# Optimization experiments

Measured on AMD Instinct MI355X. Metric: run time of the kernel, lower is better.

Reference implementation:

```python
import jax, jax.numpy as jnp
import numpy as np

N = 100000
E = 3200000
IN_DIM = 256
HID = 128
OUT_DIM = 64


def setup_inputs() -> dict:
    key = jax.random.key(0)
    ks = jax.random.split(key, 8)
    features = jax.random.normal(ks[0], (N, IN_DIM), dtype=jnp.float32)
    edge_row = jax.random.randint(ks[1], (E,), 0, N, dtype=jnp.int32)
    edge_col = jax.random.randint(ks[2], (E,), 0, N, dtype=jnp.int32)
    edge_val = jax.random.uniform(ks[3], (E,), dtype=jnp.float32)
    W1 = jax.random.normal(ks[4], (IN_DIM, HID), dtype=jnp.float32) * (1.0 / np.sqrt(IN_DIM))
    b1 = jnp.zeros((HID,), dtype=jnp.float32)
    W2 = jax.random.normal(ks[5], (HID, OUT_DIM), dtype=jnp.float32) * (1.0 / np.sqrt(HID))
    b2 = jnp.zeros((OUT_DIM,), dtype=jnp.float32)
    return {"features": features, "edge_row": edge_row, "edge_col": edge_col,
            "edge_val": edge_val, "W1": W1, "b1": b1, "W2": W2, "b2": b2}


def reference(features, edge_row, edge_col, edge_val, W1, b1, W2, b2):
    # fc1: [N, IN_DIM] @ [IN_DIM, HID] + b1
    h = features @ W1 + b1                                   # [N, HID]
    # spmm(A, h): for each edge (r, c, v): out[r] += v * h[c]
    msgs = edge_val[:, None] * h[edge_col]                    # [E, HID] gather
    h = jax.ops.segment_sum(msgs, edge_row, num_segments=N)   # [N, HID] scatter-add
    h = jax.nn.relu(h)
    h = h @ W2 + b2                                           # [N, OUT_DIM]
    return jax.nn.log_softmax(h, axis=1)
```

## Files before the change

### kernel.cpp

```cpp
#include <hip/hip_runtime.h>
#include <math.h>

constexpr int IN_DIM  = 256;
constexpr int HID     = 128;
constexpr int OUT_DIM = 64;

constexpr int BROWS   = 128;
constexpr int NBUCK   = 782;
constexpr int CAP     = 4608;
constexpr int CHUNK   = 8192;

typedef short  bf16x8 __attribute__((ext_vector_type(8)));
typedef float  f32x4  __attribute__((ext_vector_type(4)));

__device__ __forceinline__ unsigned short f2bf(float x) {
    union { float f; unsigned u; } v; v.f = x;
    unsigned r = v.u + 0x7FFF + ((v.u >> 16) & 1);
    return (unsigned short)(r >> 16);
}

__global__ __launch_bounds__(256) void w1t_kernel(const float* __restrict__ W1,
                                                  unsigned short* __restrict__ W1T)
{
    int idx = blockIdx.x * 256 + threadIdx.x;
    int k = idx >> 7;
    int n = idx & 127;
    W1T[n * IN_DIM + k] = f2bf(W1[idx]);
}

__global__ __launch_bounds__(256) void w2t_kernel(const float* __restrict__ W2,
                                                  unsigned short* __restrict__ W2T)
{
    int idx = blockIdx.x * 256 + threadIdx.x;
    int k = idx >> 6;
    int n = idx & 63;
    W2T[n * HID + k] = f2bf(W2[idx]);
}

constexpr int PADK = 264;

__global__ __launch_bounds__(256) void fc1_mfma(const float* __restrict__ feat,
                                                const unsigned short* __restrict__ W1T,
                                                const float* __restrict__ b1,
                                                unsigned short* __restrict__ h1b, int N)
{
    __shared__ unsigned short sA[64 * PADK];
    const int t    = threadIdx.x;
    const int lane = t & 63;
    const int w    = t >> 6;
    const int quad = lane >> 4;
    const int ln15 = lane & 15;
    const int row0 = blockIdx.x * 64;

#pragma unroll
    for (int i = 0; i < 16; ++i) {
        int flat = i * 256 + t;
        int r    = flat >> 6;
        int k4   = flat & 63;
        int gr   = row0 + r;
        float4 v = make_float4(0.f, 0.f, 0.f, 0.f);
        if (gr < N)
            v = *(const float4*)&feat[(size_t)gr * IN_DIM + k4 * 4];
        ushort4 o;
        o.x = f2bf(v.x); o.y = f2bf(v.y); o.z = f2bf(v.z); o.w = f2bf(v.w);
        *(ushort4*)&sA[r * PADK + k4 * 4] = o;
    }
    __syncthreads();

    f32x4 acc[8];
#pragma unroll
    for (int i = 0; i < 8; ++i) acc[i] = (f32x4){0.f, 0.f, 0.f, 0.f};

#pragma unroll
    for (int ks = 0; ks < 8; ++ks) {
        bf16x8 afrag = *(const bf16x8*)&sA[(w * 16 + ln15) * PADK + ks * 32 + quad * 8];
#pragma unroll
        for (int nt = 0; nt < 8; ++nt) {
            bf16x8 bfrag = *(const bf16x8*)&W1T[(size_t)(nt * 16 + ln15) * IN_DIM + ks * 32 + quad * 8];
            acc[nt] = __builtin_amdgcn_mfma_f32_16x16x32_bf16(afrag, bfrag, acc[nt], 0, 0, 0);
        }
    }

#pragma unroll
    for (int nt = 0; nt < 8; ++nt) {
        int col = nt * 16 + ln15;
        float bias = b1[col];
#pragma unroll
        for (int r = 0; r < 4; ++r) {
            int grow = row0 + w * 16 + quad * 4 + r;
            if (grow < N)
                h1b[(size_t)grow * HID + col] = f2bf(acc[nt][r] + bias);
        }
    }
}

__global__ __launch_bounds__(256) void bin_kernel(const int* __restrict__ erow,
                                                  const int* __restrict__ ecol,
                                                  const float* __restrict__ eval,
                                                  int* __restrict__ gCursor,
                                                  int2* __restrict__ binned, int E)
{
    __shared__ int sCnt[NBUCK];
    __shared__ int sBase[NBUCK];
    const int t = threadIdx.x;
    const int e0 = blockIdx.x * CHUNK;
    const int eEnd = min(e0 + CHUNK, E);

    for (int i = t; i < NBUCK; i += 256) sCnt[i] = 0;
    __syncthreads();

    for (int e = e0 + t; e < eEnd; e += 256)
        atomicAdd(&sCnt[erow[e] >> 7], 1);
    __syncthreads();

    for (int i = t; i < NBUCK; i += 256) {
        int c = sCnt[i];
        sBase[i] = c ? atomicAdd(&gCursor[i], c) : 0;
        sCnt[i] = 0;
    }
    __syncthreads();

    for (int e = e0 + t; e < eEnd; e += 256) {
        int   r = erow[e];
        int   c = ecol[e];
        float v = eval[e];
        int   b = r >> 7;
        int off = sBase[b] + atomicAdd(&sCnt[b], 1);
        if (off < CAP)
            binned[(size_t)b * CAP + off] = make_int2((c << 8) | ((r & 127) << 25),
                                                      __float_as_int(v));
    }
}

__global__ __launch_bounds__(256) void sort_bucket2(const int* __restrict__ gCursor,
                                                    const int2* __restrict__ binned,
                                                    int2* __restrict__ edges2,
                                                    int2* __restrict__ rowIdx, int N)
{
    __shared__ int sHist[BROWS];
    __shared__ int sStart[BROWS + 1];
    __shared__ int sCur[BROWS];
    const int t  = threadIdx.x;
    const int b  = blockIdx.x;
    const int nE = min(gCursor[b], CAP);
    const size_t base = (size_t)b * CAP;

    if (t < BROWS) sHist[t] = 0;
    __syncthreads();

    for (int i = t; i < nE; i += 256)
        atomicAdd(&sHist[(unsigned)binned[base + i].x >> 25], 1);
    __syncthreads();

    if (t < BROWS) sStart[t + 1] = sHist[t];
    if (t == 0) sStart[0] = 0;
    __syncthreads();
    for (int o = 1; o < BROWS; o <<= 1) {
        int v = 0;
        if (t < BROWS) {
            v = sStart[t + 1];
            if (t >= o) v += sStart[t + 1 - o];
        }
        __syncthreads();
        if (t < BROWS) sStart[t + 1] = v;
        __syncthreads();
    }
    if (t < BROWS) sCur[t] = sStart[t];
    __syncthreads();

    for (int i = t; i < nE; i += 256) {
        int2 p = binned[base + i];
        int rl = (unsigned)p.x >> 25;
        int pos = atomicAdd(&sCur[rl], 1);
        edges2[base + pos] = p;
    }

    if (t < BROWS) {
        int r = b * BROWS + t;
        if (r < N)
            rowIdx[r] = make_int2((int)base + sStart[t], (int)base + sStart[t + 1]);
    }
}

__device__ __forceinline__ void accum_row(const int2* __restrict__ edges2,
                                          const char* __restrict__ h1base,
                                          int j, int jend, int lane4,
                                          float& ax, float& ay)
{
    ax = 0.f; ay = 0.f;
    for (; j + 7 < jend; j += 8) {
        int2 p[8];
#pragma unroll
        for (int u = 0; u < 8; ++u) p[u] = edges2[j + u];
        unsigned g[8];
#pragma unroll
        for (int u = 0; u < 8; ++u)
            g[u] = *(const unsigned*)(h1base + ((p[u].x & 0x01FFFFFF) + lane4));
#pragma unroll
        for (int u = 0; u < 8; ++u) {
            float v = __int_as_float(p[u].y);
            ax += v * __uint_as_float(g[u] << 16);
            ay += v * __uint_as_float(g[u] & 0xFFFF0000u);
        }
    }
    for (; j < jend; ++j) {
        int2 p = edges2[j];
        unsigned g = *(const unsigned*)(h1base + ((p.x & 0x01FFFFFF) + lane4));
        float v = __int_as_float(p.y);
        ax += v * __uint_as_float(g << 16);
        ay += v * __uint_as_float(g & 0xFFFF0000u);
    }
}

__global__ __launch_bounds__(256) void spmm_kernel(const int2* __restrict__ rowIdx,
                                                   const int2* __restrict__ edges2,
                                                   const unsigned short* __restrict__ h1b,
                                                   unsigned* __restrict__ h2b, int N)
{
    const int lane  = threadIdx.x & 63;
    const int lane4 = lane * 4;
    const int wv    = (blockIdx.x * blockDim.x + threadIdx.x) >> 6;
    const int r0    = wv * 2;
    const int r1    = r0 + 1;
    if (r0 >= N) return;
    const char* h1base = (const char*)h1b;

    float ax0, ay0;
    int2 se0 = rowIdx[r0];
    accum_row(edges2, h1base, se0.x, se0.y, lane4, ax0, ay0);
    ax0 = fmaxf(ax0, 0.f); ay0 = fmaxf(ay0, 0.f);
    h2b[(size_t)r0 * 64 + lane] = (unsigned)f2bf(ax0) | ((unsigned)f2bf(ay0) << 16);

    if (r1 < N) {
        float ax1, ay1;
        int2 se1 = rowIdx[r1];
        accum_row(edges2, h1base, se1.x, se1.y, lane4, ax1, ay1);
        ax1 = fmaxf(ax1, 0.f); ay1 = fmaxf(ay1, 0.f);
        h2b[(size_t)r1 * 64 + lane] = (unsigned)f2bf(ax1) | ((unsigned)f2bf(ay1) << 16);
    }
}

__global__ __launch_bounds__(256) void fc2_mfma(const unsigned short* __restrict__ h2b,
                                                const unsigned short* __restrict__ W2T,
                                                const float* __restrict__ b2,
                                                float* __restrict__ out, int N)
{
    const int t    = threadIdx.x;
    const int lane = t & 63;
    const int w    = t >> 6;
    const int quad = lane >> 4;
    const int ln15 = lane & 15;
    const int row0 = blockIdx.x * 64;

    int arow = row0 + w * 16 + ln15;
    if (arow >= N) arow = N - 1;

    f32x4 acc[4];
#pragma unroll
    for (int i = 0; i < 4; ++i) acc[i] = (f32x4){0.f, 0.f, 0.f, 0.f};

#pragma unroll
    for (int ks = 0; ks < 4; ++ks) {
        bf16x8 afrag = *(const bf16x8*)&h2b[(size_t)arow * HID + ks * 32 + quad * 8];
#pragma unroll
        for (int nt = 0; nt < 4; ++nt) {
            bf16x8 bfrag = *(const bf16x8*)&W2T[(size_t)(nt * 16 + ln15) * HID + ks * 32 + quad * 8];
            acc[nt] = __builtin_amdgcn_mfma_f32_16x16x32_bf16(afrag, bfrag, acc[nt], 0, 0, 0);
        }
    }

    float bias[4];
#pragma unroll
    for (int nt = 0; nt < 4; ++nt) bias[nt] = b2[nt * 16 + ln15];

#pragma unroll
    for (int r = 0; r < 4; ++r) {
        float v[4];
#pragma unroll
        for (int nt = 0; nt < 4; ++nt) v[nt] = acc[nt][r] + bias[nt];

        float m = fmaxf(fmaxf(v[0], v[1]), fmaxf(v[2], v[3]));
#pragma unroll
        for (int o = 1; o < 16; o <<= 1) m = fmaxf(m, __shfl_xor(m, o));
        float s = __expf(v[0] - m) + __expf(v[1] - m) +
                  __expf(v[2] - m) + __expf(v[3] - m);
#pragma unroll
        for (int o = 1; o < 16; o <<= 1) s += __shfl_xor(s, o);
        float ls = __logf(s);

        int grow = row0 + w * 16 + quad * 4 + r;
        if (grow < N) {
#pragma unroll
            for (int nt = 0; nt < 4; ++nt)
                out[(size_t)grow * OUT_DIM + nt * 16 + ln15] = v[nt] - m - ls;
        }
    }
}

extern "C" void kernel_launch(void* const* d_in, const int* in_sizes, int n_in,
                              void* d_out, int out_size, void* d_ws, size_t ws_size,
                              hipStream_t stream) {
    const float* feat = (const float*)d_in[0];
    const int*   erow = (const int*)d_in[1];
    const int*   ecol = (const int*)d_in[2];
    const float* eval = (const float*)d_in[3];
    const float* W1   = (const float*)d_in[4];
    const float* b1   = (const float*)d_in[5];
    const float* W2   = (const float*)d_in[6];
    const float* b2   = (const float*)d_in[7];
    float*       out  = (float*)d_out;

    const int N = in_sizes[0] / IN_DIM;
    const int E = in_sizes[1];

    unsigned short* h1b    = (unsigned short*)d_ws;
    unsigned short* h2b    = h1b + (size_t)N * HID;
    int2*           binned = (int2*)(h2b + (size_t)N * HID);
    int2*           edges2 = binned + (size_t)NBUCK * CAP;
    int2*           rowIdx = edges2 + (size_t)NBUCK * CAP;
    unsigned short* W1T    = (unsigned short*)(rowIdx + N);
    unsigned short* W2T    = W1T + IN_DIM * HID;
    int*            gCursor= (int*)(W2T + HID * OUT_DIM);

    hipMemsetAsync(gCursor, 0, NBUCK * sizeof(int), stream);

    w1t_kernel<<<(IN_DIM * HID) / 256, 256, 0, stream>>>(W1, W1T);
    w2t_kernel<<<(HID * OUT_DIM) / 256, 256, 0, stream>>>(W2, W2T);
    fc1_mfma<<<(N + 63) / 64, 256, 0, stream>>>(feat, W1T, b1, h1b, N);
    bin_kernel<<<(E + CHUNK - 1) / CHUNK, 256, 0, stream>>>(erow, ecol, eval,
                                                            gCursor, binned, E);
    sort_bucket2<<<NBUCK, 256, 0, stream>>>(gCursor, binned, edges2, rowIdx, N);

    const int nwaves = (N + 1) / 2;
    const int nblk   = (nwaves + 3) / 4;
    spmm_kernel<<<nblk, 256, 0, stream>>>(rowIdx, edges2, h1b,
                                          (unsigned*)h2b, N);
    fc2_mfma<<<(N + 63) / 64, 256, 0, stream>>>(h2b, W2T, b2, out, N);
}
```

Baseline: 508.1 us.

## Fuse per-bucket edge sort into SpMM using LDS-resident sorted edges

Merges the bucket sort and SpMM kernels: each 512-thread block sorts its bucket's edges into shared memory and then has 8 waves each process 16 consecutive rows, streaming edges from LDS with a 16-way unrolled gather. This removes the global round trip for sorted edges and row indices, plus one kernel launch. It also pads gCursor counters to separate cache lines to reduce atomic contention. The risk is lower parallelism (782 blocks, with per-wave load imbalance across uneven row degrees) and a large LDS footprint limiting occupancy.

```diff
diff --git a/kernel.cpp b/kernel.cpp
--- a/kernel.cpp
+++ b/kernel.cpp
@@ -9,6 +9,7 @@
 constexpr int NBUCK   = 782;
 constexpr int CAP     = 4608;
 constexpr int CHUNK   = 8192;
+constexpr int GC_STRIDE = 16;
 
 typedef short  bf16x8 __attribute__((ext_vector_type(8)));
 typedef float  f32x4  __attribute__((ext_vector_type(4)));
@@ -115,7 +116,7 @@
 
     for (int i = t; i < NBUCK; i += 256) {
         int c = sCnt[i];
-        sBase[i] = c ? atomicAdd(&gCursor[i], c) : 0;
+        sBase[i] = c ? atomicAdd(&gCursor[i * GC_STRIDE], c) : 0;
         sCnt[i] = 0;
     }
     __syncthreads();
@@ -132,23 +133,24 @@
     }
 }
 
-__global__ __launch_bounds__(256) void sort_bucket2(const int* __restrict__ gCursor,
+__global__ __launch_bounds__(512, 6) void sort_spmm(const int* __restrict__ gCursor,
                                                     const int2* __restrict__ binned,
-                                                    int2* __restrict__ edges2,
-                                                    int2* __restrict__ rowIdx, int N)
-{
+                                                    const unsigned short* __restrict__ h1b,
+                                                    unsigned* __restrict__ h2b, int N)
+{
+    __shared__ int2 sE[CAP + 16];
     __shared__ int sHist[BROWS];
     __shared__ int sStart[BROWS + 1];
     __shared__ int sCur[BROWS];
     const int t  = threadIdx.x;
     const int b  = blockIdx.x;
-    const int nE = min(gCursor[b], CAP);
+    const int nE = min(gCursor[b * GC_STRIDE], CAP);
     const size_t base = (size_t)b * CAP;
 
     if (t < BROWS) sHist[t] = 0;
     __syncthreads();
 
-    for (int i = t; i < nE; i += 256)
+    for (int i = t; i < nE; i += 512)
         atomicAdd(&sHist[(unsigned)binned[base + i].x >> 25], 1);
     __syncthreads();
 
@@ -166,77 +168,76 @@
         __syncthreads();
     }
     if (t < BROWS) sCur[t] = sStart[t];
-    __syncthreads();
-
-    for (int i = t; i < nE; i += 256) {
+    if (t < 16) sE[nE + t] = make_int2(0, 0);
+    __syncthreads();
+
+    for (int i = t; i < nE; i += 512) {
         int2 p = binned[base + i];
         int rl = (unsigned)p.x >> 25;
         int pos = atomicAdd(&sCur[rl], 1);
-        edges2[base + pos] = p;
-    }
-
-    if (t < BROWS) {
-        int r = b * BROWS + t;
-        if (r < N)
-            rowIdx[r] = make_int2((int)base + sStart[t], (int)base + sStart[t + 1]);
-    }
-}
-
-__device__ __forceinline__ void accum_row(const int2* __restrict__ edges2,
-                                          const char* __restrict__ h1base,
-                                          int j, int jend, int lane4,
-                                          float& ax, float& ay)
-{
-    ax = 0.f; ay = 0.f;
-    for (; j + 7 < jend; j += 8) {
-        int2 p[8];
-#pragma unroll
-        for (int u = 0; u < 8; ++u) p[u] = edges2[j + u];
-        unsigned g[8];
-#pragma unroll
-        for (int u = 0; u < 8; ++u)
-            g[u] = *(const unsigned*)(h1base + ((p[u].x & 0x01FFFFFF) + lane4));
-#pragma unroll
-        for (int u = 0; u < 8; ++u) {
-            float v = __int_as_float(p[u].y);
-            ax += v * __uint_as_float(g[u] << 16);
-            ay += v * __uint_as_float(g[u] & 0xFFFF0000u);
-        }
-    }
-    for (; j < jend; ++j) {
-        int2 p = edges2[j];
-        unsigned g = *(const unsigned*)(h1base + ((p.x & 0x01FFFFFF) + lane4));
-        float v = __int_as_float(p.y);
-        ax += v * __uint_as_float(g << 16);
-        ay += v * __uint_as_float(g & 0xFFFF0000u);
-    }
-}
-
-__global__ __launch_bounds__(256) void spmm_kernel(const int2* __restrict__ rowIdx,
-                                                   const int2* __restrict__ edges2,
-                                                   const unsigned short* __restrict__ h1b,
-                                                   unsigned* __restrict__ h2b, int N)
-{
-    const int lane  = threadIdx.x & 63;
+        sE[pos] = p;
+    }
+    __syncthreads();
+
+    const int lane  = t & 63;
     const int lane4 = lane * 4;
-    const int wv    = (blockIdx.x * blockDim.x + threadIdx.x) >> 6;
-    const int r0    = wv * 2;
-    const int r1    = r0 + 1;
-    if (r0 >= N) return;
+    const int w     = t >> 6;
+    const int r0    = w * 16;
+    const int ws    = __builtin_amdgcn_readfirstlane(sStart[r0]);
+    const int we    = __builtin_amdgcn_readfirstlane(sStart[r0 + 16]);
     const char* h1base = (const char*)h1b;
-
-    float ax0, ay0;
-    int2 se0 = rowIdx[r0];
-    accum_row(edges2, h1base, se0.x, se0.y, lane4, ax0, ay0);
-    ax0 = fmaxf(ax0, 0.f); ay0 = fmaxf(ay0, 0.f);
-    h2b[(size_t)r0 * 64 + lane] = (unsigned)f2bf(ax0) | ((unsigned)f2bf(ay0) << 16);
-
-    if (r1 < N) {
-        float ax1, ay1;
-        int2 se1 = rowIdx[r1];
-        accum_row(edges2, h1base, se1.x, se1.y, lane4, ax1, ay1);
-        ax1 = fmaxf(ax1, 0.f); ay1 = fmaxf(ay1, 0.f);
-        h2b[(size_t)r1 * 64 + lane] = (unsigned)f2bf(ax1) | ((unsigned)f2bf(ay1) << 16);
+    const int gRow0 = b * BROWS;
+
+    float ax = 0.f, ay = 0.f;
+    int curRow = -1;
+
+    for (int j = ws; j < we; j += 16) {
+        int      sx[16];
+        float    vv[16];
+        unsigned g[16];
+#pragma unroll
+        for (int u = 0; u < 16; ++u) {
+            int2 e = sE[j + u];
+            sx[u] = __builtin_amdgcn_readfirstlane(e.x);
+            vv[u] = __int_as_float(e.y);
+        }
+#pragma unroll
+        for (int u = 0; u < 16; ++u)
+            g[u] = *(const unsigned*)(h1base + (sx[u] & 0x01FFFFFF) + lane4);
+#pragma unroll
+        for (int u = 0; u < 16; ++u) {
+            if (j + u < we) {
+                int nr = (int)((unsigned)sx[u] >> 25);
+                if (nr != curRow) {
+                    if (curRow >= 0) {
+                        int gr = gRow0 + curRow;
+                        if (gr < N)
+                            h2b[(size_t)gr * 64 + lane] =
+                                (unsigned)f2bf(fmaxf(ax, 0.f)) |
+                                ((unsigned)f2bf(fmaxf(ay, 0.f)) << 16);
+                    }
+                    for (int q = (curRow < 0) ? r0 : curRow + 1; q < nr; ++q) {
+                        int gr = gRow0 + q;
+                        if (gr < N) h2b[(size_t)gr * 64 + lane] = 0u;
+                    }
+                    curRow = nr; ax = 0.f; ay = 0.f;
+                }
+                float v = vv[u];
+                ax += v * __uint_as_float(g[u] << 16);
+                ay += v * __uint_as_float(g[u] & 0xFFFF0000u);
+            }
+        }
+    }
+    if (curRow >= 0) {
+        int gr = gRow0 + curRow;
+        if (gr < N)
+            h2b[(size_t)gr * 64 + lane] =
+                (unsigned)f2bf(fmaxf(ax, 0.f)) |
+                ((unsigned)f2bf(fmaxf(ay, 0.f)) << 16);
+    }
+    for (int q = (curRow < 0) ? r0 : curRow + 1; q < r0 + 16; ++q) {
+        int gr = gRow0 + q;
+        if (gr < N) h2b[(size_t)gr * 64 + lane] = 0u;
     }
 }
 
@@ -316,24 +317,18 @@
     unsigned short* h1b    = (unsigned short*)d_ws;
     unsigned short* h2b    = h1b + (size_t)N * HID;
     int2*           binned = (int2*)(h2b + (size_t)N * HID);
-    int2*           edges2 = binned + (size_t)NBUCK * CAP;
-    int2*           rowIdx = edges2 + (size_t)NBUCK * CAP;
-    unsigned short* W1T    = (unsigned short*)(rowIdx + N);
+    unsigned short* W1T    = (unsigned short*)(binned + (size_t)NBUCK * CAP);
     unsigned short* W2T    = W1T + IN_DIM * HID;
     int*            gCursor= (int*)(W2T + HID * OUT_DIM);
 
-    hipMemsetAsync(gCursor, 0, NBUCK * sizeof(int), stream);
+    hipMemsetAsync(gCursor, 0, NBUCK * GC_STRIDE * sizeof(int), stream);
 
     w1t_kernel<<<(IN_DIM * HID) / 256, 256, 0, stream>>>(W1, W1T);
     w2t_kernel<<<(HID * OUT_DIM) / 256, 256, 0, stream>>>(W2, W2T);
     fc1_mfma<<<(N + 63) / 64, 256, 0, stream>>>(feat, W1T, b1, h1b, N);
     bin_kernel<<<(E + CHUNK - 1) / CHUNK, 256, 0, stream>>>(erow, ecol, eval,
                                                             gCursor, binned, E);
-    sort_bucket2<<<NBUCK, 256, 0, stream>>>(gCursor, binned, edges2, rowIdx, N);
-
-    const int nwaves = (N + 1) / 2;
-    const int nblk   = (nwaves + 3) / 4;
-    spmm_kernel<<<nblk, 256, 0, stream>>>(rowIdx, edges2, h1b,
-                                          (unsigned*)h2b, N);
+    sort_spmm<<<NBUCK, 512, 0, stream>>>(gCursor, binned, h1b,
+                                         (unsigned*)h2b, N);
     fc2_mfma<<<(N + 63) / 64, 256, 0, stream>>>(h2b, W2T, b2, out, N);
 }
```

Result: no change. 517.9 us (+1.9%).

## Pad per-row edge lists to multiples of eight and vectorize SpMM edge loads

Applied to the files above, without the earlier changes.

The sort kernel now pads each row's edge segment to a multiple of 8 with zero-valued dummy edges, using a larger per-bucket output capacity. With that padding the SpMM loop can read edges as 16-byte nontemporal vector loads with no scalar tail loop, and it now assigns one row per wavefront instead of two. The global bucket cursors are spaced 16 ints apart to avoid atomic contention on shared cache lines. The cost is extra padding writes and workspace memory, and the dummy edges still gather h1 row 0 multiplied by zero.

```diff
diff --git a/kernel.cpp b/kernel.cpp
--- a/kernel.cpp
+++ b/kernel.cpp
@@ -8,10 +8,13 @@
 constexpr int BROWS   = 128;
 constexpr int NBUCK   = 782;
 constexpr int CAP     = 4608;
+constexpr int CAP2    = 5504;
 constexpr int CHUNK   = 8192;
+constexpr int GC_STRIDE = 16;
 
 typedef short  bf16x8 __attribute__((ext_vector_type(8)));
 typedef float  f32x4  __attribute__((ext_vector_type(4)));
+typedef int    i32x4  __attribute__((ext_vector_type(4)));
 
 __device__ __forceinline__ unsigned short f2bf(float x) {
     union { float f; unsigned u; } v; v.f = x;
@@ -115,7 +118,7 @@
 
     for (int i = t; i < NBUCK; i += 256) {
         int c = sCnt[i];
-        sBase[i] = c ? atomicAdd(&gCursor[i], c) : 0;
+        sBase[i] = c ? atomicAdd(&gCursor[i * GC_STRIDE], c) : 0;
         sCnt[i] = 0;
     }
     __syncthreads();
@@ -132,7 +135,7 @@
     }
 }
 
-__global__ __launch_bounds__(256) void sort_bucket2(const int* __restrict__ gCursor,
+__global__ __launch_bounds__(256) void sort_bucket3(const int* __restrict__ gCursor,
                                                     const int2* __restrict__ binned,
                                                     int2* __restrict__ edges2,
                                                     int2* __restrict__ rowIdx, int N)
@@ -142,17 +145,18 @@
     __shared__ int sCur[BROWS];
     const int t  = threadIdx.x;
     const int b  = blockIdx.x;
-    const int nE = min(gCursor[b], CAP);
-    const size_t base = (size_t)b * CAP;
+    const int nE = min(gCursor[b * GC_STRIDE], CAP);
+    const size_t baseIn  = (size_t)b * CAP;
+    const size_t baseOut = (size_t)b * CAP2;
 
     if (t < BROWS) sHist[t] = 0;
     __syncthreads();
 
     for (int i = t; i < nE; i += 256)
-        atomicAdd(&sHist[(unsigned)binned[base + i].x >> 25], 1);
-    __syncthreads();
-
-    if (t < BROWS) sStart[t + 1] = sHist[t];
+        atomicAdd(&sHist[(unsigned)binned[baseIn + i].x >> 25], 1);
+    __syncthreads();
+
+    if (t < BROWS) sStart[t + 1] = (sHist[t] + 7) & ~7;
     if (t == 0) sStart[0] = 0;
     __syncthreads();
     for (int o = 1; o < BROWS; o <<= 1) {
@@ -169,46 +173,21 @@
     __syncthreads();
 
     for (int i = t; i < nE; i += 256) {
-        int2 p = binned[base + i];
+        int2 p = binned[baseIn + i];
         int rl = (unsigned)p.x >> 25;
         int pos = atomicAdd(&sCur[rl], 1);
-        edges2[base + pos] = p;
+        edges2[baseOut + pos] = p;
     }
 
     if (t < BROWS) {
-        int r = b * BROWS + t;
-        if (r < N)
-            rowIdx[r] = make_int2((int)base + sStart[t], (int)base + sStart[t + 1]);
-    }
-}
-
-__device__ __forceinline__ void accum_row(const int2* __restrict__ edges2,
-                                          const char* __restrict__ h1base,
-                                          int j, int jend, int lane4,
-                                          float& ax, float& ay)
-{
-    ax = 0.f; ay = 0.f;
-    for (; j + 7 < jend; j += 8) {
-        int2 p[8];
-#pragma unroll
-        for (int u = 0; u < 8; ++u) p[u] = edges2[j + u];
-        unsigned g[8];
-#pragma unroll
-        for (int u = 0; u < 8; ++u)
-            g[u] = *(const unsigned*)(h1base + ((p[u].x & 0x01FFFFFF) + lane4));
-#pragma unroll
-        for (int u = 0; u < 8; ++u) {
-            float v = __int_as_float(p[u].y);
-            ax += v * __uint_as_float(g[u] << 16);
-            ay += v * __uint_as_float(g[u] & 0xFFFF0000u);
-        }
-    }
-    for (; j < jend; ++j) {
-        int2 p = edges2[j];
-        unsigned g = *(const unsigned*)(h1base + ((p.x & 0x01FFFFFF) + lane4));
-        float v = __int_as_float(p.y);
-        ax += v * __uint_as_float(g << 16);
-        ay += v * __uint_as_float(g & 0xFFFF0000u);
+        int h  = sHist[t];
+        int ph = (h + 7) & ~7;
+        size_t p0 = baseOut + sStart[t];
+        for (int k = h; k < ph; ++k)
+            edges2[p0 + k] = make_int2(0, 0);
+        int rr = b * BROWS + t;
+        if (rr < N)
+            rowIdx[rr] = make_int2((int)p0, (int)(p0 + ph));
     }
 }
 
@@ -219,25 +198,60 @@
 {
     const int lane  = threadIdx.x & 63;
     const int lane4 = lane * 4;
-    const int wv    = (blockIdx.x * blockDim.x + threadIdx.x) >> 6;
-    const int r0    = wv * 2;
-    const int r1    = r0 + 1;
-    if (r0 >= N) return;
+    const int r     = (blockIdx.x * blockDim.x + threadIdx.x) >> 6;
+    if (r >= N) return;
     const char* h1base = (const char*)h1b;
 
-    float ax0, ay0;
-    int2 se0 = rowIdx[r0];
-    accum_row(edges2, h1base, se0.x, se0.y, lane4, ax0, ay0);
-    ax0 = fmaxf(ax0, 0.f); ay0 = fmaxf(ay0, 0.f);
-    h2b[(size_t)r0 * 64 + lane] = (unsigned)f2bf(ax0) | ((unsigned)f2bf(ay0) << 16);
-
-    if (r1 < N) {
-        float ax1, ay1;
-        int2 se1 = rowIdx[r1];
-        accum_row(edges2, h1base, se1.x, se1.y, lane4, ax1, ay1);
-        ax1 = fmaxf(ax1, 0.f); ay1 = fmaxf(ay1, 0.f);
-        h2b[(size_t)r1 * 64 + lane] = (unsigned)f2bf(ax1) | ((unsigned)f2bf(ay1) << 16);
-    }
+    const int2 se = rowIdx[r];
+    int j = se.x;
+    const int jend = se.y;
+    float ax = 0.f, ay = 0.f;
+
+    for (; j + 16 <= jend; j += 16) {
+        i32x4 q[8];
+#pragma unroll
+        for (int u = 0; u < 8; ++u)
+            q[u] = __builtin_nontemporal_load((const i32x4*)&edges2[j + u * 2]);
+        unsigned g[16];
+#pragma unroll
+        for (int u = 0; u < 8; ++u) {
+            g[2 * u]     = *(const unsigned*)(h1base + (q[u].x & 0x01FFFFFF) + lane4);
+            g[2 * u + 1] = *(const unsigned*)(h1base + (q[u].z & 0x01FFFFFF) + lane4);
+        }
+#pragma unroll
+        for (int u = 0; u < 8; ++u) {
+            float v0 = __int_as_float(q[u].y);
+            float v1 = __int_as_float(q[u].w);
+            ax += v0 * __uint_as_float(g[2 * u] << 16);
+            ay += v0 * __uint_as_float(g[2 * u] & 0xFFFF0000u);
+            ax += v1 * __uint_as_float(g[2 * u + 1] << 16);
+            ay += v1 * __uint_as_float(g[2 * u + 1] & 0xFFFF0000u);
+        }
+    }
+    if (j < jend) {
+        i32x4 q[4];
+#pragma unroll
+        for (int u = 0; u < 4; ++u)
+            q[u] = __builtin_nontemporal_load((const i32x4*)&edges2[j + u * 2]);
+        unsigned g[8];
+#pragma unroll
+        for (int u = 0; u < 4; ++u) {
+            g[2 * u]     = *(const unsigned*)(h1base + (q[u].x & 0x01FFFFFF) + lane4);
+            g[2 * u + 1] = *(const unsigned*)(h1base + (q[u].z & 0x01FFFFFF) + lane4);
+        }
+#pragma unroll
+        for (int u = 0; u < 4; ++u) {
+            float v0 = __int_as_float(q[u].y);
+            float v1 = __int_as_float(q[u].w);
+            ax += v0 * __uint_as_float(g[2 * u] << 16);
+            ay += v0 * __uint_as_float(g[2 * u] & 0xFFFF0000u);
+            ax += v1 * __uint_as_float(g[2 * u + 1] << 16);
+            ay += v1 * __uint_as_float(g[2 * u + 1] & 0xFFFF0000u);
+        }
+    }
+
+    ax = fmaxf(ax, 0.f); ay = fmaxf(ay, 0.f);
+    h2b[(size_t)r * 64 + lane] = (unsigned)f2bf(ax) | ((unsigned)f2bf(ay) << 16);
 }
 
 __global__ __launch_bounds__(256) void fc2_mfma(const unsigned short* __restrict__ h2b,
@@ -317,22 +331,21 @@
     unsigned short* h2b    = h1b + (size_t)N * HID;
     int2*           binned = (int2*)(h2b + (size_t)N * HID);
     int2*           edges2 = binned + (size_t)NBUCK * CAP;
-    int2*           rowIdx = edges2 + (size_t)NBUCK * CAP;
+    int2*           rowIdx = edges2 + (size_t)NBUCK * CAP2;
     unsigned short* W1T    = (unsigned short*)(rowIdx + N);
     unsigned short* W2T    = W1T + IN_DIM * HID;
     int*            gCursor= (int*)(W2T + HID * OUT_DIM);
 
-    hipMemsetAsync(gCursor, 0, NBUCK * sizeof(int), stream);
+    hipMemsetAsync(gCursor, 0, NBUCK * GC_STRIDE * sizeof(int), stream);
 
     w1t_kernel<<<(IN_DIM * HID) / 256, 256, 0, stream>>>(W1, W1T);
     w2t_kernel<<<(HID * OUT_DIM) / 256, 256, 0, stream>>>(W2, W2T);
     fc1_mfma<<<(N + 63) / 64, 256, 0, stream>>>(feat, W1T, b1, h1b, N);
     bin_kernel<<<(E + CHUNK - 1) / CHUNK, 256, 0, stream>>>(erow, ecol, eval,
                                                             gCursor, binned, E);
-    sort_bucket2<<<NBUCK, 256, 0, stream>>>(gCursor, binned, edges2, rowIdx, N);
-
-    const int nwaves = (N + 1) / 2;
-    const int nblk   = (nwaves + 3) / 4;
+    sort_bucket3<<<NBUCK, 256, 0, stream>>>(gCursor, binned, edges2, rowIdx, N);
+
+    const int nblk = (N + 3) / 4;
     spmm_kernel<<<nblk, 256, 0, stream>>>(rowIdx, edges2, h1b,
                                           (unsigned*)h2b, N);
     fc2_mfma<<<(N + 63) / 64, 256, 0, stream>>>(h2b, W2T, b2, out, N);
```

New measurement: 515.3 us. No clear change (+1.4%).
